# Performance work log

Hardware: AMD Instinct MI355X
Metric: run time of the kernel (lower is better)

## Reference

```python
import jax, jax.numpy as jnp
import numpy as np

N, E = 16000, 256000
IN_DIM, HID, OUT_DIM, NH = 128, 128, 128, 16
HD = OUT_DIM // NH  # 8
EDGE_F, R_F = 4, 20
KV_IN = 2 * IN_DIM + EDGE_F + R_F  # 280
EPS = 1e-5
INV_SQRT_HD = float(1.0 / np.sqrt(HD))


def _ln(x, g, b):
    mu = jnp.mean(x, -1, keepdims=True)
    var = jnp.mean(jnp.square(x - mu), -1, keepdims=True)
    return (x - mu) * jax.lax.rsqrt(var + EPS) * g + b


def _mlp(x, W1, b1, g, be, W2, b2):
    # Linear -> LayerNorm -> ReLU -> Linear (targetdiff-style 2-layer MLP)
    hdn = jax.nn.relu(_ln(x @ W1 + b1, g, be))
    return hdn @ W2 + b2


def setup_inputs() -> dict:
    key = jax.random.key(0)
    k = jax.random.split(key, 16)
    s = 0.02
    f32 = jnp.float32
    return {
        "h": jax.random.normal(k[0], (N, IN_DIM), f32),
        "rel_x": jax.random.normal(k[1], (E, 3), f32),
        "r_feat": jax.random.uniform(k[2], (E, R_F), f32),
        "edge_feat": jax.random.normal(k[3], (E, EDGE_F), f32),
        "edge_index": jax.random.randint(k[4], (2, E), 0, N),
        # xk MLP: KV_IN -> HID -> OUT_DIM
        "xk_W1": jax.random.normal(k[5], (KV_IN, HID), f32) * s,
        "xk_b1": jnp.zeros((HID,), f32),
        "xk_g": jnp.ones((HID,), f32),
        "xk_be": jnp.zeros((HID,), f32),
        "xk_W2": jax.random.normal(k[6], (HID, OUT_DIM), f32) * s,
        "xk_b2": jnp.zeros((OUT_DIM,), f32),
        # xv MLP: KV_IN -> HID -> NH
        "xv_W1": jax.random.normal(k[7], (KV_IN, HID), f32) * s,
        "xv_b1": jnp.zeros((HID,), f32),
        "xv_g": jnp.ones((HID,), f32),
        "xv_be": jnp.zeros((HID,), f32),
        "xv_W2": jax.random.normal(k[8], (HID, NH), f32) * s,
        "xv_b2": jnp.zeros((NH,), f32),
        # xq MLP: IN_DIM -> HID -> OUT_DIM
        "xq_W1": jax.random.normal(k[9], (IN_DIM, HID), f32) * s,
        "xq_b1": jnp.zeros((HID,), f32),
        "xq_g": jnp.ones((HID,), f32),
        "xq_be": jnp.zeros((HID,), f32),
        "xq_W2": jax.random.normal(k[10], (HID, OUT_DIM), f32) * s,
        "xq_b2": jnp.zeros((OUT_DIM,), f32),
        # ew_net: Linear(R_F, 1) + sigmoid
        "ew_W": jax.random.normal(k[11], (R_F, 1), f32) * s,
        "ew_b": jnp.zeros((1,), f32),
    }


def reference(h, rel_x, r_feat, edge_feat, edge_index,
              xk_W1, xk_b1, xk_g, xk_be, xk_W2, xk_b2,
              xv_W1, xv_b1, xv_g, xv_be, xv_W2, xv_b2,
              xq_W1, xq_b1, xq_g, xq_be, xq_W2, xq_b2,
              ew_W, ew_b):
    n = h.shape[0]
    src, dst = edge_index[0], edge_index[1]
    hi, hj = h[dst], h[src]                                    # [E, IN_DIM] each
    kv_input = jnp.concatenate([edge_feat, r_feat, hi, hj], -1)  # [E, KV_IN]
    k = _mlp(kv_input, xk_W1, xk_b1, xk_g, xk_be, xk_W2, xk_b2).reshape(-1, NH, HD)
    v = _mlp(kv_input, xv_W1, xv_b1, xv_g, xv_be, xv_W2, xv_b2)  # [E, NH]
    e_w = jax.nn.sigmoid(r_feat @ ew_W + ew_b)                   # [E, 1]
    v = v * e_w
    v = v[:, :, None] * rel_x[:, None, :]                        # [E, NH, 3]
    q = _mlp(h, xq_W1, xq_b1, xq_g, xq_be, xq_W2, xq_b2).reshape(-1, NH, HD)
    scores = jnp.sum(q[dst] * k, -1) * INV_SQRT_HD               # [E, NH]
    # scatter_softmax over dst groups (numerically stable)
    smax = jax.lax.stop_gradient(jax.ops.segment_max(scores, dst, num_segments=n))
    ex = jnp.exp(scores - smax[dst])
    denom = jax.ops.segment_sum(ex, dst, num_segments=n)
    alpha = ex / denom[dst]                                      # [E, NH]
    m = alpha[:, :, None] * v                                    # [E, NH, 3]
    out = jax.ops.segment_sum(m, dst, num_segments=n)            # [N, NH, 3]
    return out.mean(1)                                           # [N, 3]
```

## Files before the change

### kernel.cpp

```cpp
#include <hip/hip_runtime.h>
#include <math.h>

#define NN 16000
#define NE 256000
#define INV_SQRT_HD 0.35355339059327373f
#define LN_EPS 1e-5f

typedef __attribute__((ext_vector_type(8))) short bf16x8;
typedef __attribute__((ext_vector_type(4))) float f32x4;
typedef _Float16 half8_ __attribute__((ext_vector_type(8)));
typedef _Float16 half4_ __attribute__((ext_vector_type(4)));

__device__ inline unsigned short f2bf(float x) {
    unsigned u = __float_as_uint(x);
    unsigned r = ((u >> 16) & 1u) + 0x7FFFu;
    return (unsigned short)((u + r) >> 16);
}
__device__ inline float bf2f(unsigned short u) {
    return __uint_as_float(((unsigned)u) << 16);
}

__global__ __launch_bounds__(256) void prep_kernel(
    const float* __restrict__ h,
    const float* __restrict__ r_feat,
    const float* __restrict__ edge_feat,
    const float* __restrict__ ewW, const float* __restrict__ ewB,
    const float* __restrict__ kW1, const float* __restrict__ vW1,
    const float* __restrict__ kW2, const float* __restrict__ vW2,
    const float* __restrict__ qW1, const float* __restrict__ qW2,
    unsigned short* __restrict__ h_bf, unsigned short* __restrict__ feats_bf,
    float* __restrict__ ew_pre,
    unsigned short* __restrict__ w1fp, unsigned short* __restrict__ w1d,
    unsigned short* __restrict__ w1s,  unsigned short* __restrict__ w2p,
    unsigned short* __restrict__ w1q,  unsigned short* __restrict__ w2q)
{
    const int b = blockIdx.x, t = threadIdx.x;
    if (b < 1000) {
        const int gid = b * 256 + t;
        const float4* hp = (const float4*)(h + (size_t)gid * 8);
        float4 a = hp[0], c = hp[1];
        ushort4 u0, u1;
        u0.x = f2bf(a.x); u0.y = f2bf(a.y); u0.z = f2bf(a.z); u0.w = f2bf(a.w);
        u1.x = f2bf(c.x); u1.y = f2bf(c.y); u1.z = f2bf(c.z); u1.w = f2bf(c.w);
        *(ushort4*)(h_bf + (size_t)gid * 8) = u0;
        *(ushort4*)(h_bf + (size_t)gid * 8 + 4) = u1;
    } else if (b < 2000) {
        const int e = (b - 1000) * 256 + t;
        float4 ef = *(const float4*)(edge_feat + (size_t)e * 4);
        float rf[20];
        #pragma unroll
        for (int i = 0; i < 5; ++i)
            *(float4*)&rf[i * 4] = *(const float4*)(r_feat + (size_t)e * 20 + i * 4);
        float z = ewB[0];
        #pragma unroll
        for (int i = 0; i < 20; ++i) z = fmaf(rf[i], ewW[i], z);
        ew_pre[e] = (1.f / (1.f + expf(-z))) * (1.f / 16.f);
        unsigned short fb[32];
        fb[0] = f2bf(ef.x); fb[1] = f2bf(ef.y); fb[2] = f2bf(ef.z); fb[3] = f2bf(ef.w);
        #pragma unroll
        for (int i = 0; i < 20; ++i) fb[4 + i] = f2bf(rf[i]);
        #pragma unroll
        for (int i = 24; i < 32; ++i) fb[i] = 0;
        #pragma unroll
        for (int i = 0; i < 4; ++i)
            *(int4*)(feats_bf + (size_t)e * 32 + i * 8) = *(int4*)&fb[i * 8];
    } else {
        const int idx = (b - 2000) * 256 + t;
        if (idx < 8192) {
            int j = idx & 7, l = (idx >> 3) & 63, mtc = (idx >> 9) & 15;
            int kp = (l >> 4) * 8 + j;
            int col = mtc * 16 + (l & 15);
            float v = 0.f;
            if (kp < 24) v = (col < 128) ? kW1[(size_t)kp * 128 + col]
                                         : vW1[(size_t)kp * 128 + col - 128];
            w1fp[idx] = f2bf(v);
        } else if (idx < 40960) {
            int i = idx - 8192;
            int j = i & 7, l = (i >> 3) & 63, mt = (i >> 9) & 15, s = i >> 13;
            int k = s * 32 + (l >> 4) * 8 + j;
            int col = mt * 16 + (l & 15);
            int row = 24 + k;
            float v = (col < 128) ? kW1[(size_t)row * 128 + col]
                                  : vW1[(size_t)row * 128 + col - 128];
            w1d[i] = f2bf(v);
        } else if (idx < 73728) {
            int i = idx - 40960;
            int j = i & 7, l = (i >> 3) & 63, mt = (i >> 9) & 15, s = i >> 13;
            int k = s * 32 + (l >> 4) * 8 + j;
            int col = mt * 16 + (l & 15);
            int row = 152 + k;
            float v = (col < 128) ? kW1[(size_t)row * 128 + col]
                                  : vW1[(size_t)row * 128 + col - 128];
            w1s[i] = f2bf(v);
        } else if (idx < 92160) {
            int i2 = idx - 73728;
            int j = i2 & 7, l = (i2 >> 3) & 63, sc = i2 >> 9;
            int ct = sc % 9, s2 = sc / 9;
            int k = s2 * 32 + (l >> 4) * 8 + j;
            float v = (ct < 8) ? kW2[(size_t)k * 128 + ct * 16 + (l & 15)]
                               : vW2[(size_t)k * 16 + (l & 15)];
            w2p[i2] = f2bf(v);
        } else if (idx < 108544) {
            int i3 = idx - 92160;
            int j = i3 & 7, l = (i3 >> 3) & 63, mt = (i3 >> 9) & 7, s = i3 >> 12;
            int k = s * 32 + (l >> 4) * 8 + j;
            w1q[i3] = f2bf(qW1[(size_t)k * 128 + mt * 16 + (l & 15)]);
        } else if (idx < 124928) {
            int i4 = idx - 108544;
            int j = i4 & 7, l = (i4 >> 3) & 63, mt = (i4 >> 9) & 7, s = i4 >> 12;
            int k = s * 32 + (l >> 4) * 8 + j;
            w2q[i4] = f2bf(qW2[(size_t)k * 128 + mt * 16 + (l & 15)]);
        }
    }
}

__global__ __launch_bounds__(256, 2) void hprep_kernel(
    const unsigned short* __restrict__ h_bf,
    const unsigned short* __restrict__ w1d, const unsigned short* __restrict__ w1s,
    unsigned short* __restrict__ Hd, unsigned short* __restrict__ Hs)
{
    const int t = threadIdx.x, nb = blockIdx.x * 32;
    const int wc = t >> 6, l = t & 63, lrow = l & 15, lgrp = l >> 4;

    unsigned offN[2];
    #pragma unroll
    for (int nt = 0; nt < 2; ++nt)
        offN[nt] = (unsigned)(nb + nt * 16 + lrow) * 128 + lgrp * 8;

    f32x4 ad[4][2], as2[4][2];
    #pragma unroll
    for (int mt = 0; mt < 4; ++mt)
        #pragma unroll
        for (int nt = 0; nt < 2; ++nt) {
            ad[mt][nt][0] = 0.f; ad[mt][nt][1] = 0.f; ad[mt][nt][2] = 0.f; ad[mt][nt][3] = 0.f;
            as2[mt][nt][0] = 0.f; as2[mt][nt][1] = 0.f; as2[mt][nt][2] = 0.f; as2[mt][nt][3] = 0.f;
        }
    {
        auto ldA = [&](int s, bf16x8* dD, bf16x8* dS) {
            #pragma unroll
            for (int mt = 0; mt < 4; ++mt) {
                dD[mt] = *(const bf16x8*)(w1d + (size_t)((s * 16 + wc * 4 + mt) * 64 + l) * 8);
                dS[mt] = *(const bf16x8*)(w1s + (size_t)((s * 16 + wc * 4 + mt) * 64 + l) * 8);
            }
        };
        auto ldB = [&](int s, bf16x8* dst) {
            #pragma unroll
            for (int nt = 0; nt < 2; ++nt)
                dst[nt] = *(const bf16x8*)(h_bf + offN[nt] + s * 32);
        };
        bf16x8 aD[2][4], aS[2][4], bB[2][2];
        ldA(0, aD[0], aS[0]); ldB(0, bB[0]);
        ldA(1, aD[1], aS[1]); ldB(1, bB[1]);
        #pragma unroll
        for (int s = 0; s < 4; ++s) {
            const int c = s & 1;
            #pragma unroll
            for (int mt = 0; mt < 4; ++mt)
                #pragma unroll
                for (int nt = 0; nt < 2; ++nt) {
                    ad[mt][nt]  = __builtin_amdgcn_mfma_f32_16x16x32_bf16(aD[c][mt], bB[c][nt], ad[mt][nt], 0, 0, 0);
                    as2[mt][nt] = __builtin_amdgcn_mfma_f32_16x16x32_bf16(aS[c][mt], bB[c][nt], as2[mt][nt], 0, 0, 0);
                }
            if (s < 2) { ldA(s + 2, aD[c], aS[c]); ldB(s + 2, bB[c]); }
        }
    }
    #pragma unroll
    for (int mt = 0; mt < 4; ++mt) {
        const int cb = wc * 64 + mt * 16 + lgrp * 4;
        #pragma unroll
        for (int nt = 0; nt < 2; ++nt) {
            const int el = nt * 16 + lrow;
            half4_ od, os;
            od[0] = (_Float16)ad[mt][nt][0]; od[1] = (_Float16)ad[mt][nt][1];
            od[2] = (_Float16)ad[mt][nt][2]; od[3] = (_Float16)ad[mt][nt][3];
            os[0] = (_Float16)as2[mt][nt][0]; os[1] = (_Float16)as2[mt][nt][1];
            os[2] = (_Float16)as2[mt][nt][2]; os[3] = (_Float16)as2[mt][nt][3];
            *(half4_*)(Hd + (size_t)(nb + el) * 256 + cb) = od;
            *(half4_*)(Hs + (size_t)(nb + el) * 256 + cb) = os;
        }
    }
}

__global__ __launch_bounds__(256, 4) void qmlp_kernel(
    const unsigned short* __restrict__ h_bf,
    const float* __restrict__ B1, const float* __restrict__ G,
    const float* __restrict__ BE, const float* __restrict__ B2,
    const unsigned short* __restrict__ w1q, const unsigned short* __restrict__ w2q,
    unsigned short* __restrict__ q_bf)
{
    __shared__ __align__(16) unsigned char hsq[8192];
    __shared__ float2 lnb[4][32];
    __shared__ float  gb1[128];
    __shared__ float2 gbe[128];
    __shared__ float  gb2[128];

    const int t = threadIdx.x;
    const int nb = blockIdx.x * 32;
    const int wc = t >> 6, l = t & 63, lrow = l & 15, lgrp = l >> 4;

    if (t < 128) { gb1[t] = B1[t]; gbe[t] = make_float2(G[t], BE[t]); gb2[t] = B2[t]; }

    unsigned offN[2];
    #pragma unroll
    for (int nt = 0; nt < 2; ++nt)
        offN[nt] = (unsigned)(nb + nt * 16 + lrow) * 128 + lgrp * 8;
    __syncthreads();

    f32x4 acc1[2][2];
    #pragma unroll
    for (int mt = 0; mt < 2; ++mt) {
        const int cb = wc * 32 + mt * 16 + lgrp * 4;
        #pragma unroll
        for (int nt = 0; nt < 2; ++nt) {
            acc1[mt][nt][0] = gb1[cb];     acc1[mt][nt][1] = gb1[cb + 1];
            acc1[mt][nt][2] = gb1[cb + 2]; acc1[mt][nt][3] = gb1[cb + 3];
        }
    }
    {
        auto ldA = [&](int s, bf16x8* dst) {
            #pragma unroll
            for (int mt = 0; mt < 2; ++mt)
                dst[mt] = *(const bf16x8*)(w1q + (size_t)((s * 8 + wc * 2 + mt) * 64 + l) * 8);
        };
        auto ldB = [&](int s, bf16x8* dst) {
            #pragma unroll
            for (int nt = 0; nt < 2; ++nt)
                dst[nt] = *(const bf16x8*)(h_bf + offN[nt] + s * 32);
        };
        bf16x8 aB[2][2], bB[2][2];
        ldA(0, aB[0]); ldB(0, bB[0]);
        ldA(1, aB[1]); ldB(1, bB[1]);
        #pragma unroll
        for (int s = 0; s < 4; ++s) {
            const int c = s & 1;
            #pragma unroll
            for (int mt = 0; mt < 2; ++mt)
                #pragma unroll
                for (int nt = 0; nt < 2; ++nt)
                    acc1[mt][nt] = __builtin_amdgcn_mfma_f32_16x16x32_bf16(aB[c][mt], bB[c][nt], acc1[mt][nt], 0, 0, 0);
            if (s < 2) { ldA(s + 2, aB[c]); ldB(s + 2, bB[c]); }
        }
    }

    float2 myln[2];
    #pragma unroll
    for (int nt = 0; nt < 2; ++nt) {
        float p1 = 0.f, p2 = 0.f;
        #pragma unroll
        for (int mt = 0; mt < 2; ++mt)
            #pragma unroll
            for (int r = 0; r < 4; ++r) { float v = acc1[mt][nt][r]; p1 += v; p2 += v * v; }
        p1 += __shfl_xor(p1, 16); p2 += __shfl_xor(p2, 16);
        p1 += __shfl_xor(p1, 32); p2 += __shfl_xor(p2, 32);
        myln[nt] = make_float2(p1, p2);
        if (l < 16) lnb[wc][nt * 16 + l] = myln[nt];
    }
    __syncthreads();

    #pragma unroll
    for (int nt = 0; nt < 2; ++nt) {
        const int el = nt * 16 + lrow;
        float2 a0 = lnb[0][el], a1 = lnb[1][el], a2 = lnb[2][el], a3 = lnb[3][el];
        const float s1 = a0.x + a1.x + a2.x + a3.x;
        const float s2 = a0.y + a1.y + a2.y + a3.y;
        const float mu = s1 * (1.f / 128.f);
        const float rs = rsqrtf(s2 * (1.f / 128.f) - mu * mu + LN_EPS);
        #pragma unroll
        for (int mt = 0; mt < 2; ++mt) {
            const int cb = wc * 32 + mt * 16 + lgrp * 4;
            const float2 g0 = gbe[cb], g1 = gbe[cb+1], g2 = gbe[cb+2], g3 = gbe[cb+3];
            ushort4 u;
            u.x = f2bf(fmaxf((acc1[mt][nt][0] - mu) * rs * g0.x + g0.y, 0.f));
            u.y = f2bf(fmaxf((acc1[mt][nt][1] - mu) * rs * g1.x + g1.y, 0.f));
            u.z = f2bf(fmaxf((acc1[mt][nt][2] - mu) * rs * g2.x + g2.y, 0.f));
            u.w = f2bf(fmaxf((acc1[mt][nt][3] - mu) * rs * g3.x + g3.y, 0.f));
            *(ushort4*)(hsq + ((cb >> 3) * 32 + el) * 16 + (lgrp & 1) * 8) = u;
        }
    }
    __syncthreads();

    f32x4 acc2[2][2];
    #pragma unroll
    for (int km = 0; km < 2; ++km) {
        const int c2 = (wc * 2 + km) * 16 + lgrp * 4;
        #pragma unroll
        for (int nt = 0; nt < 2; ++nt) {
            acc2[km][nt][0] = gb2[c2];     acc2[km][nt][1] = gb2[c2 + 1];
            acc2[km][nt][2] = gb2[c2 + 2]; acc2[km][nt][3] = gb2[c2 + 3];
        }
    }
    {
        bf16x8 a0C = *(const bf16x8*)(w2q + (size_t)((wc * 2) * 64 + l) * 8);
        bf16x8 a1C = *(const bf16x8*)(w2q + (size_t)((wc * 2 + 1) * 64 + l) * 8);
        #pragma unroll
        for (int s2 = 0; s2 < 4; ++s2) {
            bf16x8 a0N, a1N;
            if (s2 < 3) {
                a0N = *(const bf16x8*)(w2q + (size_t)(((s2+1) * 8 + wc * 2) * 64 + l) * 8);
                a1N = *(const bf16x8*)(w2q + (size_t)(((s2+1) * 8 + wc * 2 + 1) * 64 + l) * 8);
            }
            bf16x8 hb[2];
            #pragma unroll
            for (int nt = 0; nt < 2; ++nt)
                hb[nt] = *(const bf16x8*)(hsq + (((s2 * 4 + lgrp) * 32) + nt * 16 + lrow) * 16);
            #pragma unroll
            for (int nt = 0; nt < 2; ++nt) {
                acc2[0][nt] = __builtin_amdgcn_mfma_f32_16x16x32_bf16(a0C, hb[nt], acc2[0][nt], 0, 0, 0);
                acc2[1][nt] = __builtin_amdgcn_mfma_f32_16x16x32_bf16(a1C, hb[nt], acc2[1][nt], 0, 0, 0);
            }
            a0C = a0N; a1C = a1N;
        }
    }
    #pragma unroll
    for (int km = 0; km < 2; ++km) {
        const int c2 = (wc * 2 + km) * 16 + lgrp * 4;
        #pragma unroll
        for (int nt = 0; nt < 2; ++nt) {
            const int el = nt * 16 + lrow;
            ushort4 o;
            o.x = f2bf(acc2[km][nt][0]); o.y = f2bf(acc2[km][nt][1]);
            o.z = f2bf(acc2[km][nt][2]); o.w = f2bf(acc2[km][nt][3]);
            *(ushort4*)(q_bf + (size_t)(nb + el) * 128 + c2) = o;
        }
    }
}

__global__ __launch_bounds__(256, 3) void edge_kernel(
    const unsigned short* __restrict__ feats_bf,
    const int*   __restrict__ eidx,
    const float* __restrict__ ew_pre,
    const unsigned short* __restrict__ Hd, const unsigned short* __restrict__ Hs,
    const float* __restrict__ kB1, const float* __restrict__ kG, const float* __restrict__ kBE,
    const float* __restrict__ vB1, const float* __restrict__ vG, const float* __restrict__ vBE,
    const float* __restrict__ kB2, const float* __restrict__ vB2,
    const unsigned short* __restrict__ w1fp, const unsigned short* __restrict__ w2p,
    const unsigned short* __restrict__ q_bf,
    float* __restrict__ ex_out, float* __restrict__ vw_out, float* __restrict__ denom)
{
    __shared__ __align__(16) unsigned char xs[16384];
    __shared__ __align__(16) unsigned char hs[16384];
    __shared__ float2 lnb[4][32];
    __shared__ float  gb1[256];
    __shared__ float2 gbe[256];
    __shared__ float  gb2[144];
    __shared__ float  ew_s[32];

    const int t = threadIdx.x;
    const int eb = blockIdx.x * 32;
    const int wc = t >> 6, l = t & 63, lrow = l & 15, lgrp = l >> 4;

    const int el0 = t & 31;
    const int c0  = t >> 5;
    const int dste = eidx[NE + eb + el0];
    const int srce = eidx[eb + el0];
    half8_ sd[4], ss[4];
    #pragma unroll
    for (int r = 0; r < 4; ++r) {
        const int c = r * 8 + c0;
        sd[r] = *(const half8_*)(Hd + (size_t)dste * 256 + c * 8);
        ss[r] = *(const half8_*)(Hs + (size_t)srce * 256 + c * 8);
    }

    bf16x8 bF[2];
    int dst01[2];
    #pragma unroll
    for (int nt = 0; nt < 2; ++nt) {
        const int e = eb + nt * 16 + lrow;
        bF[nt] = *(const bf16x8*)(feats_bf + (size_t)e * 32 + lgrp * 8);
        dst01[nt] = eidx[NE + e];
    }
    int2 qreg[2][2];
    #pragma unroll
    for (int km = 0; km < 2; ++km)
        #pragma unroll
        for (int nt = 0; nt < 2; ++nt)
            qreg[km][nt] = *(const int2*)(q_bf + (size_t)dst01[nt] * 128 + (wc * 2 + km) * 16 + lgrp * 4);
    bf16x8 aF[4];
    #pragma unroll
    for (int mt = 0; mt < 4; ++mt)
        aF[mt] = *(const bf16x8*)(w1fp + (size_t)((wc * 4 + mt) * 64 + l) * 8);

    gb1[t] = (t < 128) ? kB1[t] : vB1[t - 128];
    gbe[t] = make_float2((t < 128) ? kG[t] : vG[t - 128],
                         (t < 128) ? kBE[t] : vBE[t - 128]);
    if (t < 144) gb2[t] = (t < 128) ? kB2[t] : vB2[t - 128];
    if (t < 32) ew_s[t] = ew_pre[eb + t];

    #pragma unroll
    for (int r = 0; r < 4; ++r) {
        const int c = r * 8 + c0;
        *(half8_*)(xs + (c * 32 + el0) * 16) = sd[r] + ss[r];
    }
    __syncthreads();

    f32x4 acc1[4][2];
    #pragma unroll
    for (int mt = 0; mt < 4; ++mt) {
        const int cb = wc * 64 + mt * 16 + lgrp * 4;
        #pragma unroll
        for (int nt = 0; nt < 2; ++nt) {
            acc1[mt][nt][0] = gb1[cb];     acc1[mt][nt][1] = gb1[cb + 1];
            acc1[mt][nt][2] = gb1[cb + 2]; acc1[mt][nt][3] = gb1[cb + 3];
        }
    }
    #pragma unroll
    for (int mt = 0; mt < 4; ++mt)
        #pragma unroll
        for (int nt = 0; nt < 2; ++nt)
            acc1[mt][nt] = __builtin_amdgcn_mfma_f32_16x16x32_bf16(aF[mt], bF[nt], acc1[mt][nt], 0, 0, 0);

    #pragma unroll
    for (int mt = 0; mt < 4; ++mt) {
        const int cb = wc * 64 + mt * 16 + lgrp * 4;
        const int chunk = cb >> 3;
        const int hoff = (lgrp & 1) * 8;
        #pragma unroll
        for (int nt = 0; nt < 2; ++nt) {
            const int el = nt * 16 + lrow;
            half4_ hv = *(const half4_*)(xs + (chunk * 32 + el) * 16 + hoff);
            acc1[mt][nt][0] += (float)hv[0];
            acc1[mt][nt][1] += (float)hv[1];
            acc1[mt][nt][2] += (float)hv[2];
            acc1[mt][nt][3] += (float)hv[3];
        }
    }

    float2 myln[2];
    #pragma unroll
    for (int nt = 0; nt < 2; ++nt) {
        float p1 = 0.f, p2 = 0.f;
        #pragma unroll
        for (int mt = 0; mt < 4; ++mt)
            #pragma unroll
            for (int r = 0; r < 4; ++r) { float v = acc1[mt][nt][r]; p1 += v; p2 += v * v; }
        p1 += __shfl_xor(p1, 16); p2 += __shfl_xor(p2, 16);
        p1 += __shfl_xor(p1, 32); p2 += __shfl_xor(p2, 32);
        myln[nt] = make_float2(p1, p2);
        if (l < 16) lnb[wc][nt * 16 + l] = myln[nt];
    }
    __syncthreads();

    #pragma unroll
    for (int nt = 0; nt < 2; ++nt) {
        const int el = nt * 16 + lrow;
        const float2 oth = lnb[wc ^ 1][el];
        const float s1 = myln[nt].x + oth.x, s2 = myln[nt].y + oth.y;
        const float mu = s1 * (1.f / 128.f);
        const float rs = rsqrtf(s2 * (1.f / 128.f) - mu * mu + LN_EPS);
        #pragma unroll
        for (int mt = 0; mt < 4; ++mt) {
            const int cb = wc * 64 + mt * 16 + lgrp * 4;
            const int region = cb >> 7, kc = cb & 127;
            const float2 g0 = gbe[cb], g1 = gbe[cb+1], g2 = gbe[cb+2], g3 = gbe[cb+3];
            ushort4 u;
            u.x = f2bf(fmaxf((acc1[mt][nt][0] - mu) * rs * g0.x + g0.y, 0.f));
            u.y = f2bf(fmaxf((acc1[mt][nt][1] - mu) * rs * g1.x + g1.y, 0.f));
            u.z = f2bf(fmaxf((acc1[mt][nt][2] - mu) * rs * g2.x + g2.y, 0.f));
            u.w = f2bf(fmaxf((acc1[mt][nt][3] - mu) * rs * g3.x + g3.y, 0.f));
            *(ushort4*)(hs + region * 8192 + ((kc >> 3) * 32 + el) * 16 + (lgrp & 1) * 8) = u;
        }
    }
    __syncthreads();

    f32x4 acc2[2][2], accv;
    #pragma unroll
    for (int km = 0; km < 2; ++km) {
        const int c0b = (wc * 2 + km) * 16 + lgrp * 4;
        #pragma unroll
        for (int nt = 0; nt < 2; ++nt) {
            acc2[km][nt][0] = gb2[c0b];     acc2[km][nt][1] = gb2[c0b + 1];
            acc2[km][nt][2] = gb2[c0b + 2]; acc2[km][nt][3] = gb2[c0b + 3];
        }
    }
    const int vel = wc * 16 + lrow;
    {
        const int cv = 128 + lgrp * 4;
        accv[0] = gb2[cv]; accv[1] = gb2[cv+1]; accv[2] = gb2[cv+2]; accv[3] = gb2[cv+3];
    }
    {
        bf16x8 a0C = *(const bf16x8*)(w2p + (size_t)((wc * 2) * 64 + l) * 8);
        bf16x8 a1C = *(const bf16x8*)(w2p + (size_t)((wc * 2 + 1) * 64 + l) * 8);
        bf16x8 avC = *(const bf16x8*)(w2p + (size_t)(8 * 64 + l) * 8);
        #pragma unroll
        for (int s2 = 0; s2 < 4; ++s2) {
            bf16x8 a0N, a1N, avN;
            if (s2 < 3) {
                a0N = *(const bf16x8*)(w2p + (size_t)(((s2+1) * 9 + wc * 2) * 64 + l) * 8);
                a1N = *(const bf16x8*)(w2p + (size_t)(((s2+1) * 9 + wc * 2 + 1) * 64 + l) * 8);
                avN = *(const bf16x8*)(w2p + (size_t)(((s2+1) * 9 + 8) * 64 + l) * 8);
            }
            bf16x8 hb[2];
            #pragma unroll
            for (int nt = 0; nt < 2; ++nt)
                hb[nt] = *(const bf16x8*)(hs + ((s2 * 4 + lgrp) * 32 + nt * 16 + lrow) * 16);
            #pragma unroll
            for (int nt = 0; nt < 2; ++nt) {
                acc2[0][nt] = __builtin_amdgcn_mfma_f32_16x16x32_bf16(a0C, hb[nt], acc2[0][nt], 0, 0, 0);
                acc2[1][nt] = __builtin_amdgcn_mfma_f32_16x16x32_bf16(a1C, hb[nt], acc2[1][nt], 0, 0, 0);
            }
            if (wc < 2) {
                bf16x8 hv = *(const bf16x8*)(hs + 8192 + ((s2 * 4 + lgrp) * 32 + vel) * 16);
                accv = __builtin_amdgcn_mfma_f32_16x16x32_bf16(avC, hv, accv, 0, 0, 0);
            }
            a0C = a0N; a1C = a1N; avC = avN;
        }
    }

    if (wc < 2) {
        const float sc = ew_s[vel];
        float4 vo;
        vo.x = accv[0] * sc; vo.y = accv[1] * sc; vo.z = accv[2] * sc; vo.w = accv[3] * sc;
        *(float4*)(vw_out + (size_t)(eb + vel) * 16 + lgrp * 4) = vo;
    }

    #pragma unroll
    for (int km = 0; km < 2; ++km) {
        #pragma unroll
        for (int nt = 0; nt < 2; ++nt) {
            const int el = nt * 16 + lrow;
            const int2 qv = qreg[km][nt];
            const float q0 = bf2f((unsigned short)(qv.x & 0xffff));
            const float q1 = bf2f((unsigned short)(((unsigned)qv.x) >> 16));
            const float q2 = bf2f((unsigned short)(qv.y & 0xffff));
            const float q3 = bf2f((unsigned short)(((unsigned)qv.y) >> 16));
            float sp = acc2[km][nt][0] * q0 + acc2[km][nt][1] * q1
                     + acc2[km][nt][2] * q2 + acc2[km][nt][3] * q3;
            sp += __shfl_xor(sp, 16);
            if ((l & 16) == 0) {
                const float exv = expf(sp * INV_SQRT_HD);
                const int hh = (wc * 2 + km) * 2 + (lgrp >> 1);
                ex_out[(size_t)(eb + el) * 16 + hh] = exv;
                atomicAdd(&denom[(size_t)dst01[nt] * 16 + hh], exv);
            }
        }
    }
}

__global__ __launch_bounds__(256) void finalize_kernel(
    const int* __restrict__ eidx, const float* __restrict__ relx,
    const float* __restrict__ exb, const float* __restrict__ vwb,
    const float* __restrict__ den, float* __restrict__ out)
{
    const int e = blockIdx.x * 256 + threadIdx.x;
    const int dst = eidx[NE + e];
    const float4* ex4 = (const float4*)(exb + (size_t)e*16);
    const float4* vw4 = (const float4*)(vwb + (size_t)e*16);
    const float4* dn4 = (const float4*)(den + (size_t)dst*16);
    float s = 0.f;
    #pragma unroll
    for (int k = 0; k < 4; ++k) {
        float4 a = ex4[k], b = vw4[k], d = dn4[k];
        s += (a.x/d.x)*b.x + (a.y/d.y)*b.y + (a.z/d.z)*b.z + (a.w/d.w)*b.w;
    }
    float r0 = relx[(size_t)e*3+0], r1 = relx[(size_t)e*3+1], r2 = relx[(size_t)e*3+2];
    atomicAdd(&out[(size_t)dst*3+0], s*r0);
    atomicAdd(&out[(size_t)dst*3+1], s*r1);
    atomicAdd(&out[(size_t)dst*3+2], s*r2);
}

extern "C" void kernel_launch(void* const* d_in, const int* in_sizes, int n_in,
                              void* d_out, int out_size, void* d_ws, size_t ws_size,
                              hipStream_t stream) {
    const float* h         = (const float*)d_in[0];
    const float* rel_x     = (const float*)d_in[1];
    const float* r_feat    = (const float*)d_in[2];
    const float* edge_feat = (const float*)d_in[3];
    const int*   eidx      = (const int*)  d_in[4];
    const float* kW1 = (const float*)d_in[5];
    const float* kB1 = (const float*)d_in[6];
    const float* kG  = (const float*)d_in[7];
    const float* kBE = (const float*)d_in[8];
    const float* kW2 = (const float*)d_in[9];
    const float* kB2 = (const float*)d_in[10];
    const float* vW1 = (const float*)d_in[11];
    const float* vB1 = (const float*)d_in[12];
    const float* vG  = (const float*)d_in[13];
    const float* vBE = (const float*)d_in[14];
    const float* vW2 = (const float*)d_in[15];
    const float* vB2 = (const float*)d_in[16];
    const float* qW1 = (const float*)d_in[17];
    const float* qB1 = (const float*)d_in[18];
    const float* qG  = (const float*)d_in[19];
    const float* qBE = (const float*)d_in[20];
    const float* qW2 = (const float*)d_in[21];
    const float* qB2 = (const float*)d_in[22];
    const float* ewW = (const float*)d_in[23];
    const float* ewB = (const float*)d_in[24];

    float* ws   = (float*)d_ws;
    float* qbuf = ws;
    float* exb  = qbuf + (size_t)NN*128;
    float* vwb  = exb + (size_t)NE*16;
    float* den  = vwb + (size_t)NE*16;
    float* ewp  = den + (size_t)NN*16;
    unsigned short* w1fp = (unsigned short*)(ewp + (size_t)NE);
    unsigned short* w1d  = w1fp + 8192;
    unsigned short* w1s  = w1d + 32768;
    unsigned short* w2p  = w1s + 32768;
    unsigned short* w1q  = w2p + 18432;
    unsigned short* w2q  = w1q + 16384;
    unsigned short* h_bf = w2q + 16384;
    unsigned short* feats_bf = h_bf + (size_t)NN*128;
    unsigned short* Hd   = feats_bf + (size_t)NE*32;
    unsigned short* Hs   = Hd + (size_t)NN*256;
    unsigned short* q_bf = (unsigned short*)qbuf;
    float* outf = (float*)d_out;

    hipMemsetAsync(den, 0, (size_t)NN*16*sizeof(float), stream);
    hipMemsetAsync(outf, 0, (size_t)NN*3*sizeof(float), stream);

    prep_kernel<<<2488, 256, 0, stream>>>(h, r_feat, edge_feat, ewW, ewB,
                                          kW1, vW1, kW2, vW2, qW1, qW2,
                                          h_bf, feats_bf, ewp,
                                          w1fp, w1d, w1s, w2p, w1q, w2q);
    hprep_kernel<<<NN/32, 256, 0, stream>>>(h_bf, w1d, w1s, Hd, Hs);
    qmlp_kernel<<<NN/32, 256, 0, stream>>>(h_bf, qB1, qG, qBE, qB2, w1q, w2q, q_bf);
    edge_kernel<<<NE/32, 256, 0, stream>>>(feats_bf, eidx, ewp,
                                           Hd, Hs,
                                           kB1, kG, kBE, vB1, vG, vBE,
                                           kB2, vB2, w1fp, w2p, q_bf,
                                           exb, vwb, den);
    finalize_kernel<<<NE/256, 256, 0, stream>>>(eidx, rel_x, exb, vwb, den, outf);
}
```

Measured before the change: 228.0 us.

## Gather node projections directly into MFMA layout and drop LDS staging in edge kernel

The edge kernel no longer stages the summed dst/src node projections in a 16 KB shared buffer. Each lane now gathers the half4 slices it needs straight into registers in the MFMA accumulator layout, which removes one __syncthreads and the LDS traffic. Bias, gamma/beta and edge-weight values are read directly from global memory as float4 instead of being staged in shared arrays, and the prep kernel stages r_feat/edge_feat through LDS so its global loads are coalesced. The cost is more scattered, smaller gathers per lane and more live registers, which can hurt latency hiding.

```diff
diff --git a/kernel.cpp b/kernel.cpp
--- a/kernel.cpp
+++ b/kernel.cpp
@@ -34,6 +34,7 @@
     unsigned short* __restrict__ w1s,  unsigned short* __restrict__ w2p,
     unsigned short* __restrict__ w1q,  unsigned short* __restrict__ w2q)
 {
+    __shared__ float stage[6144];
     const int b = blockIdx.x, t = threadIdx.x;
     if (b < 1000) {
         const int gid = b * 256 + t;
@@ -45,18 +46,27 @@
         *(ushort4*)(h_bf + (size_t)gid * 8) = u0;
         *(ushort4*)(h_bf + (size_t)gid * 8 + 4) = u1;
     } else if (b < 2000) {
-        const int e = (b - 1000) * 256 + t;
-        float4 ef = *(const float4*)(edge_feat + (size_t)e * 4);
+        const int eb2 = (b - 1000) * 256;
+        float* rfs = stage;
+        float* efs = stage + 5120;
+        #pragma unroll
+        for (int i = 0; i < 5; ++i) {
+            const int idx = i * 1024 + t * 4;
+            *(float4*)&rfs[idx] = *(const float4*)(r_feat + (size_t)eb2 * 20 + idx);
+        }
+        *(float4*)&efs[t * 4] = *(const float4*)(edge_feat + (size_t)eb2 * 4 + t * 4);
+        __syncthreads();
+        const int e = eb2 + t;
         float rf[20];
         #pragma unroll
-        for (int i = 0; i < 5; ++i)
-            *(float4*)&rf[i * 4] = *(const float4*)(r_feat + (size_t)e * 20 + i * 4);
+        for (int i = 0; i < 20; ++i) rf[i] = rfs[t * 20 + i];
         float z = ewB[0];
         #pragma unroll
         for (int i = 0; i < 20; ++i) z = fmaf(rf[i], ewW[i], z);
         ew_pre[e] = (1.f / (1.f + expf(-z))) * (1.f / 16.f);
         unsigned short fb[32];
-        fb[0] = f2bf(ef.x); fb[1] = f2bf(ef.y); fb[2] = f2bf(ef.z); fb[3] = f2bf(ef.w);
+        fb[0] = f2bf(efs[t*4+0]); fb[1] = f2bf(efs[t*4+1]);
+        fb[2] = f2bf(efs[t*4+2]); fb[3] = f2bf(efs[t*4+3]);
         #pragma unroll
         for (int i = 0; i < 20; ++i) fb[4 + i] = f2bf(rf[i]);
         #pragma unroll
@@ -337,70 +347,57 @@
     const unsigned short* __restrict__ q_bf,
     float* __restrict__ ex_out, float* __restrict__ vw_out, float* __restrict__ denom)
 {
-    __shared__ __align__(16) unsigned char xs[16384];
     __shared__ __align__(16) unsigned char hs[16384];
     __shared__ float2 lnb[4][32];
-    __shared__ float  gb1[256];
-    __shared__ float2 gbe[256];
-    __shared__ float  gb2[144];
-    __shared__ float  ew_s[32];
 
     const int t = threadIdx.x;
     const int eb = blockIdx.x * 32;
     const int wc = t >> 6, l = t & 63, lrow = l & 15, lgrp = l >> 4;
 
-    const int el0 = t & 31;
-    const int c0  = t >> 5;
-    const int dste = eidx[NE + eb + el0];
-    const int srce = eidx[eb + el0];
-    half8_ sd[4], ss[4];
-    #pragma unroll
-    for (int r = 0; r < 4; ++r) {
-        const int c = r * 8 + c0;
-        sd[r] = *(const half8_*)(Hd + (size_t)dste * 256 + c * 8);
-        ss[r] = *(const half8_*)(Hs + (size_t)srce * 256 + c * 8);
-    }
-
-    bf16x8 bF[2];
-    int dst01[2];
+    int dst01[2], src01[2];
     #pragma unroll
     for (int nt = 0; nt < 2; ++nt) {
         const int e = eb + nt * 16 + lrow;
-        bF[nt] = *(const bf16x8*)(feats_bf + (size_t)e * 32 + lgrp * 8);
         dst01[nt] = eidx[NE + e];
-    }
+        src01[nt] = eidx[e];
+    }
+
+    half4_ ghd[4][2], ghs[4][2];
+    #pragma unroll
+    for (int mt = 0; mt < 4; ++mt) {
+        const int cb = wc * 64 + mt * 16 + lgrp * 4;
+        #pragma unroll
+        for (int nt = 0; nt < 2; ++nt) {
+            ghd[mt][nt] = *(const half4_*)(Hd + (size_t)dst01[nt] * 256 + cb);
+            ghs[mt][nt] = *(const half4_*)(Hs + (size_t)src01[nt] * 256 + cb);
+        }
+    }
+
+    bf16x8 bF[2];
+    #pragma unroll
+    for (int nt = 0; nt < 2; ++nt)
+        bF[nt] = *(const bf16x8*)(feats_bf + (size_t)(eb + nt * 16 + lrow) * 32 + lgrp * 8);
+    bf16x8 aF[4];
+    #pragma unroll
+    for (int mt = 0; mt < 4; ++mt)
+        aF[mt] = *(const bf16x8*)(w1fp + (size_t)((wc * 4 + mt) * 64 + l) * 8);
     int2 qreg[2][2];
     #pragma unroll
     for (int km = 0; km < 2; ++km)
         #pragma unroll
         for (int nt = 0; nt < 2; ++nt)
             qreg[km][nt] = *(const int2*)(q_bf + (size_t)dst01[nt] * 128 + (wc * 2 + km) * 16 + lgrp * 4);
-    bf16x8 aF[4];
-    #pragma unroll
-    for (int mt = 0; mt < 4; ++mt)
-        aF[mt] = *(const bf16x8*)(w1fp + (size_t)((wc * 4 + mt) * 64 + l) * 8);
-
-    gb1[t] = (t < 128) ? kB1[t] : vB1[t - 128];
-    gbe[t] = make_float2((t < 128) ? kG[t] : vG[t - 128],
-                         (t < 128) ? kBE[t] : vBE[t - 128]);
-    if (t < 144) gb2[t] = (t < 128) ? kB2[t] : vB2[t - 128];
-    if (t < 32) ew_s[t] = ew_pre[eb + t];
-
-    #pragma unroll
-    for (int r = 0; r < 4; ++r) {
-        const int c = r * 8 + c0;
-        *(half8_*)(xs + (c * 32 + el0) * 16) = sd[r] + ss[r];
-    }
-    __syncthreads();
 
     f32x4 acc1[4][2];
     #pragma unroll
     for (int mt = 0; mt < 4; ++mt) {
         const int cb = wc * 64 + mt * 16 + lgrp * 4;
-        #pragma unroll
-        for (int nt = 0; nt < 2; ++nt) {
-            acc1[mt][nt][0] = gb1[cb];     acc1[mt][nt][1] = gb1[cb + 1];
-            acc1[mt][nt][2] = gb1[cb + 2]; acc1[mt][nt][3] = gb1[cb + 3];
+        const float4 b1 = (cb < 128) ? *(const float4*)(kB1 + cb)
+                                     : *(const float4*)(vB1 + cb - 128);
+        #pragma unroll
+        for (int nt = 0; nt < 2; ++nt) {
+            acc1[mt][nt][0] = b1.x; acc1[mt][nt][1] = b1.y;
+            acc1[mt][nt][2] = b1.z; acc1[mt][nt][3] = b1.w;
         }
     }
     #pragma unroll
@@ -408,22 +405,15 @@
         #pragma unroll
         for (int nt = 0; nt < 2; ++nt)
             acc1[mt][nt] = __builtin_amdgcn_mfma_f32_16x16x32_bf16(aF[mt], bF[nt], acc1[mt][nt], 0, 0, 0);
-
-    #pragma unroll
-    for (int mt = 0; mt < 4; ++mt) {
-        const int cb = wc * 64 + mt * 16 + lgrp * 4;
-        const int chunk = cb >> 3;
-        const int hoff = (lgrp & 1) * 8;
-        #pragma unroll
-        for (int nt = 0; nt < 2; ++nt) {
-            const int el = nt * 16 + lrow;
-            half4_ hv = *(const half4_*)(xs + (chunk * 32 + el) * 16 + hoff);
-            acc1[mt][nt][0] += (float)hv[0];
-            acc1[mt][nt][1] += (float)hv[1];
-            acc1[mt][nt][2] += (float)hv[2];
-            acc1[mt][nt][3] += (float)hv[3];
-        }
-    }
+    #pragma unroll
+    for (int mt = 0; mt < 4; ++mt)
+        #pragma unroll
+        for (int nt = 0; nt < 2; ++nt) {
+            acc1[mt][nt][0] += (float)ghd[mt][nt][0] + (float)ghs[mt][nt][0];
+            acc1[mt][nt][1] += (float)ghd[mt][nt][1] + (float)ghs[mt][nt][1];
+            acc1[mt][nt][2] += (float)ghd[mt][nt][2] + (float)ghs[mt][nt][2];
+            acc1[mt][nt][3] += (float)ghd[mt][nt][3] + (float)ghs[mt][nt][3];
+        }
 
     float2 myln[2];
     #pragma unroll
@@ -451,12 +441,13 @@
         for (int mt = 0; mt < 4; ++mt) {
             const int cb = wc * 64 + mt * 16 + lgrp * 4;
             const int region = cb >> 7, kc = cb & 127;
-            const float2 g0 = gbe[cb], g1 = gbe[cb+1], g2 = gbe[cb+2], g3 = gbe[cb+3];
+            const float4 g4  = (cb < 128) ? *(const float4*)(kG + cb)  : *(const float4*)(vG + cb - 128);
+            const float4 be4 = (cb < 128) ? *(const float4*)(kBE + cb) : *(const float4*)(vBE + cb - 128);
             ushort4 u;
-            u.x = f2bf(fmaxf((acc1[mt][nt][0] - mu) * rs * g0.x + g0.y, 0.f));
-            u.y = f2bf(fmaxf((acc1[mt][nt][1] - mu) * rs * g1.x + g1.y, 0.f));
-            u.z = f2bf(fmaxf((acc1[mt][nt][2] - mu) * rs * g2.x + g2.y, 0.f));
-            u.w = f2bf(fmaxf((acc1[mt][nt][3] - mu) * rs * g3.x + g3.y, 0.f));
+            u.x = f2bf(fmaxf((acc1[mt][nt][0] - mu) * rs * g4.x + be4.x, 0.f));
+            u.y = f2bf(fmaxf((acc1[mt][nt][1] - mu) * rs * g4.y + be4.y, 0.f));
+            u.z = f2bf(fmaxf((acc1[mt][nt][2] - mu) * rs * g4.z + be4.z, 0.f));
+            u.w = f2bf(fmaxf((acc1[mt][nt][3] - mu) * rs * g4.w + be4.w, 0.f));
             *(ushort4*)(hs + region * 8192 + ((kc >> 3) * 32 + el) * 16 + (lgrp & 1) * 8) = u;
         }
     }
@@ -466,16 +457,17 @@
     #pragma unroll
     for (int km = 0; km < 2; ++km) {
         const int c0b = (wc * 2 + km) * 16 + lgrp * 4;
-        #pragma unroll
-        for (int nt = 0; nt < 2; ++nt) {
-            acc2[km][nt][0] = gb2[c0b];     acc2[km][nt][1] = gb2[c0b + 1];
-            acc2[km][nt][2] = gb2[c0b + 2]; acc2[km][nt][3] = gb2[c0b + 3];
+        const float4 b2 = *(const float4*)(kB2 + c0b);
+        #pragma unroll
+        for (int nt = 0; nt < 2; ++nt) {
+            acc2[km][nt][0] = b2.x; acc2[km][nt][1] = b2.y;
+            acc2[km][nt][2] = b2.z; acc2[km][nt][3] = b2.w;
         }
     }
     const int vel = wc * 16 + lrow;
     {
-        const int cv = 128 + lgrp * 4;
-        accv[0] = gb2[cv]; accv[1] = gb2[cv+1]; accv[2] = gb2[cv+2]; accv[3] = gb2[cv+3];
+        const float4 bv = *(const float4*)(vB2 + lgrp * 4);
+        accv[0] = bv.x; accv[1] = bv.y; accv[2] = bv.z; accv[3] = bv.w;
     }
     {
         bf16x8 a0C = *(const bf16x8*)(w2p + (size_t)((wc * 2) * 64 + l) * 8);
@@ -507,7 +499,7 @@
     }
 
     if (wc < 2) {
-        const float sc = ew_s[vel];
+        const float sc = ew_pre[eb + vel];
         float4 vo;
         vo.x = accv[0] * sc; vo.y = accv[1] * sc; vo.z = accv[2] * sc; vo.w = accv[3] * sc;
         *(float4*)(vw_out + (size_t)(eb + vel) * 16 + lgrp * 4) = vo;
```

After: 248.4 us. +9.0%, slower.

## Coalesce edge gathers, stage q rows in LDS, alias x/h shared buffers

Applied to the files above, without the earlier changes.

In the edge kernel, the Hd/Hs row gathers are reorganised so 8 consecutive threads read contiguous 16-byte chunks of one row. The q row for each destination is now fetched as whole 256-byte rows into a padded LDS buffer instead of as scattered 8-byte register loads. The x and h shared buffers are merged into one region, which lowers the LDS footprint and may allow more blocks per CU. The prep kernel also stages r_feat and edge_feat through shared memory so the global reads are coalesced. The cost is extra LDS traffic and an added barrier in the prep kernel.

```diff
diff --git a/kernel.cpp b/kernel.cpp
--- a/kernel.cpp
+++ b/kernel.cpp
@@ -34,6 +34,7 @@
     unsigned short* __restrict__ w1s,  unsigned short* __restrict__ w2p,
     unsigned short* __restrict__ w1q,  unsigned short* __restrict__ w2q)
 {
+    __shared__ float stage[6144];
     const int b = blockIdx.x, t = threadIdx.x;
     if (b < 1000) {
         const int gid = b * 256 + t;
@@ -45,18 +46,27 @@
         *(ushort4*)(h_bf + (size_t)gid * 8) = u0;
         *(ushort4*)(h_bf + (size_t)gid * 8 + 4) = u1;
     } else if (b < 2000) {
-        const int e = (b - 1000) * 256 + t;
-        float4 ef = *(const float4*)(edge_feat + (size_t)e * 4);
+        const int eb2 = (b - 1000) * 256;
+        float* rfs = stage;
+        float* efs = stage + 5120;
+        #pragma unroll
+        for (int i = 0; i < 5; ++i) {
+            const int idx = i * 1024 + t * 4;
+            *(float4*)&rfs[idx] = *(const float4*)(r_feat + (size_t)eb2 * 20 + idx);
+        }
+        *(float4*)&efs[t * 4] = *(const float4*)(edge_feat + (size_t)eb2 * 4 + t * 4);
+        __syncthreads();
+        const int e = eb2 + t;
         float rf[20];
         #pragma unroll
-        for (int i = 0; i < 5; ++i)
-            *(float4*)&rf[i * 4] = *(const float4*)(r_feat + (size_t)e * 20 + i * 4);
+        for (int i = 0; i < 20; ++i) rf[i] = rfs[t * 20 + i];
         float z = ewB[0];
         #pragma unroll
         for (int i = 0; i < 20; ++i) z = fmaf(rf[i], ewW[i], z);
         ew_pre[e] = (1.f / (1.f + expf(-z))) * (1.f / 16.f);
         unsigned short fb[32];
-        fb[0] = f2bf(ef.x); fb[1] = f2bf(ef.y); fb[2] = f2bf(ef.z); fb[3] = f2bf(ef.w);
+        fb[0] = f2bf(efs[t*4+0]); fb[1] = f2bf(efs[t*4+1]);
+        fb[2] = f2bf(efs[t*4+2]); fb[3] = f2bf(efs[t*4+3]);
         #pragma unroll
         for (int i = 0; i < 20; ++i) fb[4 + i] = f2bf(rf[i]);
         #pragma unroll
@@ -337,8 +347,8 @@
     const unsigned short* __restrict__ q_bf,
     float* __restrict__ ex_out, float* __restrict__ vw_out, float* __restrict__ denom)
 {
-    __shared__ __align__(16) unsigned char xs[16384];
-    __shared__ __align__(16) unsigned char hs[16384];
+    __shared__ __align__(16) unsigned char xhs[16384];
+    __shared__ __align__(16) unsigned char qs[8448];
     __shared__ float2 lnb[4][32];
     __shared__ float  gb1[256];
     __shared__ float2 gbe[256];
@@ -349,16 +359,25 @@
     const int eb = blockIdx.x * 32;
     const int wc = t >> 6, l = t & 63, lrow = l & 15, lgrp = l >> 4;
 
-    const int el0 = t & 31;
-    const int c0  = t >> 5;
-    const int dste = eidx[NE + eb + el0];
-    const int srce = eidx[eb + el0];
-    half8_ sd[4], ss[4];
-    #pragma unroll
-    for (int r = 0; r < 4; ++r) {
-        const int c = r * 8 + c0;
-        sd[r] = *(const half8_*)(Hd + (size_t)dste * 256 + c * 8);
-        ss[r] = *(const half8_*)(Hs + (size_t)srce * 256 + c * 8);
+    const int el8 = t >> 3;
+    const int ch8 = t & 7;
+    const int d8 = eidx[NE + eb + el8];
+    const int s8 = eidx[eb + el8];
+    int4 gd[4], gs4[4];
+    #pragma unroll
+    for (int p = 0; p < 4; ++p)
+        gd[p] = *(const int4*)(Hd + (size_t)d8 * 256 + (p * 8 + ch8) * 8);
+    #pragma unroll
+    for (int p = 0; p < 4; ++p)
+        gs4[p] = *(const int4*)(Hs + (size_t)s8 * 256 + (p * 8 + ch8) * 8);
+
+    int4 gq[2]; int elq[2];
+    #pragma unroll
+    for (int m = 0; m < 2; ++m) {
+        elq[m] = m * 16 + (t >> 4);
+        const int chq = t & 15;
+        const int dq = eidx[NE + eb + elq[m]];
+        gq[m] = *(const int4*)(q_bf + (size_t)dq * 128 + chq * 8);
     }
 
     bf16x8 bF[2];
@@ -369,12 +388,6 @@
         bF[nt] = *(const bf16x8*)(feats_bf + (size_t)e * 32 + lgrp * 8);
         dst01[nt] = eidx[NE + e];
     }
-    int2 qreg[2][2];
-    #pragma unroll
-    for (int km = 0; km < 2; ++km)
-        #pragma unroll
-        for (int nt = 0; nt < 2; ++nt)
-            qreg[km][nt] = *(const int2*)(q_bf + (size_t)dst01[nt] * 128 + (wc * 2 + km) * 16 + lgrp * 4);
     bf16x8 aF[4];
     #pragma unroll
     for (int mt = 0; mt < 4; ++mt)
@@ -387,10 +400,15 @@
     if (t < 32) ew_s[t] = ew_pre[eb + t];
 
     #pragma unroll
-    for (int r = 0; r < 4; ++r) {
-        const int c = r * 8 + c0;
-        *(half8_*)(xs + (c * 32 + el0) * 16) = sd[r] + ss[r];
-    }
+    for (int p = 0; p < 4; ++p) {
+        const int chunk = p * 8 + ch8;
+        half8_ a = __builtin_bit_cast(half8_, gd[p]);
+        half8_ b = __builtin_bit_cast(half8_, gs4[p]);
+        *(half8_*)(xhs + (chunk * 32 + el8) * 16) = a + b;
+    }
+    #pragma unroll
+    for (int m = 0; m < 2; ++m)
+        *(int4*)(qs + elq[m] * 264 + (t & 15) * 16) = gq[m];
     __syncthreads();
 
     f32x4 acc1[4][2];
@@ -417,7 +435,7 @@
         #pragma unroll
         for (int nt = 0; nt < 2; ++nt) {
             const int el = nt * 16 + lrow;
-            half4_ hv = *(const half4_*)(xs + (chunk * 32 + el) * 16 + hoff);
+            half4_ hv = *(const half4_*)(xhs + (chunk * 32 + el) * 16 + hoff);
             acc1[mt][nt][0] += (float)hv[0];
             acc1[mt][nt][1] += (float)hv[1];
             acc1[mt][nt][2] += (float)hv[2];
@@ -457,7 +475,7 @@
             u.y = f2bf(fmaxf((acc1[mt][nt][1] - mu) * rs * g1.x + g1.y, 0.f));
             u.z = f2bf(fmaxf((acc1[mt][nt][2] - mu) * rs * g2.x + g2.y, 0.f));
             u.w = f2bf(fmaxf((acc1[mt][nt][3] - mu) * rs * g3.x + g3.y, 0.f));
-            *(ushort4*)(hs + region * 8192 + ((kc >> 3) * 32 + el) * 16 + (lgrp & 1) * 8) = u;
+            *(ushort4*)(xhs + region * 8192 + ((kc >> 3) * 32 + el) * 16 + (lgrp & 1) * 8) = u;
         }
     }
     __syncthreads();
@@ -492,14 +510,14 @@
             bf16x8 hb[2];
             #pragma unroll
             for (int nt = 0; nt < 2; ++nt)
-                hb[nt] = *(const bf16x8*)(hs + ((s2 * 4 + lgrp) * 32 + nt * 16 + lrow) * 16);
+                hb[nt] = *(const bf16x8*)(xhs + ((s2 * 4 + lgrp) * 32 + nt * 16 + lrow) * 16);
             #pragma unroll
             for (int nt = 0; nt < 2; ++nt) {
                 acc2[0][nt] = __builtin_amdgcn_mfma_f32_16x16x32_bf16(a0C, hb[nt], acc2[0][nt], 0, 0, 0);
                 acc2[1][nt] = __builtin_amdgcn_mfma_f32_16x16x32_bf16(a1C, hb[nt], acc2[1][nt], 0, 0, 0);
             }
             if (wc < 2) {
-                bf16x8 hv = *(const bf16x8*)(hs + 8192 + ((s2 * 4 + lgrp) * 32 + vel) * 16);
+                bf16x8 hv = *(const bf16x8*)(xhs + 8192 + ((s2 * 4 + lgrp) * 32 + vel) * 16);
                 accv = __builtin_amdgcn_mfma_f32_16x16x32_bf16(avC, hv, accv, 0, 0, 0);
             }
             a0C = a0N; a1C = a1N; avC = avN;
@@ -518,7 +536,8 @@
         #pragma unroll
         for (int nt = 0; nt < 2; ++nt) {
             const int el = nt * 16 + lrow;
-            const int2 qv = qreg[km][nt];
+            const int c0 = (wc * 2 + km) * 16 + lgrp * 4;
+            const int2 qv = *(const int2*)(qs + el * 264 + c0 * 2);
             const float q0 = bf2f((unsigned short)(qv.x & 0xffff));
             const float q1 = bf2f((unsigned short)(((unsigned)qv.x) >> 16));
             const float q2 = bf2f((unsigned short)(qv.y & 0xffff));
```

After: 220.4 us. 3.3% less time.
